# Optimization experiments

Hardware: AMD Instinct MI355X
Metric: run time of the kernel (lower is better)

## Reference

```python
import jax, jax.numpy as jnp
import numpy as np

B, C, T = 4, 768, 512
H, KS, NL, W = 12, 3, 6, 4
D = C // H  # 64


def setup_inputs() -> dict:
    key = jax.random.key(0)
    ks = jax.random.split(key, 24)
    def n(k, shape, scale):
        return jax.random.normal(k, shape, dtype=jnp.float32) * scale
    cscale = C ** -0.5
    return {
        "x": jax.random.normal(ks[0], (B, C, T), dtype=jnp.float32),
        "x_mask": jnp.ones((B, 1, T), dtype=jnp.float32),
        "Wq": n(ks[1], (NL, C, C), cscale), "bq": jnp.zeros((NL, C), jnp.float32),
        "Wk": n(ks[2], (NL, C, C), cscale), "bk": jnp.zeros((NL, C), jnp.float32),
        "Wv": n(ks[3], (NL, C, C), cscale), "bv": jnp.zeros((NL, C), jnp.float32),
        "Wo": n(ks[4], (NL, C, C), cscale), "bo": jnp.zeros((NL, C), jnp.float32),
        "emb_rel_k": n(ks[5], (NL, D, 2 * W + 1), D ** -0.5),
        "emb_rel_v": n(ks[6], (NL, D, 2 * W + 1), D ** -0.5),
        "ffn_w1": n(ks[7], (NL, 4 * C, C, KS), (C * KS) ** -0.5),
        "ffn_b1": jnp.zeros((NL, 4 * C), jnp.float32),
        "ffn_w2": n(ks[8], (NL, C, 4 * C, KS), (4 * C * KS) ** -0.5),
        "ffn_b2": jnp.zeros((NL, C), jnp.float32),
        "norm1_g": jnp.ones((NL, C), jnp.float32), "norm1_b": jnp.zeros((NL, C), jnp.float32),
        "norm2_g": jnp.ones((NL, C), jnp.float32), "norm2_b": jnp.zeros((NL, C), jnp.float32),
    }


def _conv1x1(x, w, b):  # x:[B,C,T] w:[O,C] -> [B,O,T]
    return jnp.einsum('oc,bct->bot', w, x) + b[None, :, None]


def _conv1d(x, w, b, pad):  # x:[B,Ci,T] w:[O,Ci,K]
    y = jax.lax.conv_general_dilated(x, w, (1,), [(pad, pad)],
                                     dimension_numbers=('NCH', 'OIH', 'NCH'))
    return y + b[None, :, None]


def _layer_norm_c(x, g, b):  # normalize over channel dim of [B,C,T]
    m = jnp.mean(x, axis=1, keepdims=True)
    v = jnp.var(x, axis=1, keepdims=True)
    return (x - m) * jax.lax.rsqrt(v + 1e-5) * g[None, :, None] + b[None, :, None]


def _rel_to_abs(x):  # [b,h,l,2l-1] -> [b,h,l,l]
    b, h, l, _ = x.shape
    x = jnp.pad(x, ((0, 0), (0, 0), (0, 0), (0, 1)))
    x = x.reshape(b, h, l * 2 * l)
    x = jnp.pad(x, ((0, 0), (0, 0), (0, l - 1)))
    return x.reshape(b, h, l + 1, 2 * l - 1)[:, :, :l, l - 1:]


def _abs_to_rel(x):  # [b,h,l,l] -> [b,h,l,2l-1]
    b, h, l, _ = x.shape
    x = jnp.pad(x, ((0, 0), (0, 0), (0, 0), (0, l - 1)))
    x = x.reshape(b, h, l * l + l * (l - 1))
    x = jnp.pad(x, ((0, 0), (0, 0), (l, 0)))
    return x.reshape(b, h, l, 2 * l)[:, :, :, 1:]


def _get_rel_emb(emb, t, w):  # emb:[D,2w+1] -> [D,2t-1]
    pad = max(t - (w + 1), 0)
    start = max(w + 1 - t, 0)
    e = jnp.pad(emb, ((0, 0), (pad, pad)))
    return e[:, start:start + 2 * t - 1]


def _attention(x, attn_mask, wq, bq, wk, bk, wv, bv, wo, bo, ek, ev):
    b, c, t = x.shape
    scale = D ** 0.5
    q = _conv1x1(x, wq, bq).reshape(b, H, D, t)
    k = _conv1x1(x, wk, bk).reshape(b, H, D, t)
    v = _conv1x1(x, wv, bv).reshape(b, H, D, t)
    scores = jnp.einsum('bhdt,bhds->bhts', q, k) / scale  # [b,H,t,t]
    k_emb = _get_rel_emb(ek, t, W)  # [D,2t-1]
    rel_logits = jnp.einsum('bhdt,dr->bhtr', q / scale, k_emb)
    scores = scores + _rel_to_abs(rel_logits)
    scores = jnp.where(attn_mask == 0, -10000.0, scores)
    p = jax.nn.softmax(scores, axis=-1)
    out = jnp.einsum('bhts,bhds->bhdt', p, v)
    v_emb = _get_rel_emb(ev, t, W)  # [D,2t-1]
    out = out + jnp.einsum('bhtr,dr->bhdt', _abs_to_rel(p), v_emb)
    return _conv1x1(out.reshape(b, c, t), wo, bo)


def _ffn(x, x_mask, w1, b1, w2, b2):
    y = _conv1d(x * x_mask, w1, b1, KS // 2)
    y = jax.nn.gelu(y, approximate=False)
    y = _conv1d(y * x_mask, w2, b2, KS // 2)
    return y * x_mask


def reference(x, x_mask, Wq, bq, Wk, bk, Wv, bv, Wo, bo, emb_rel_k, emb_rel_v,
              ffn_w1, ffn_b1, ffn_w2, ffn_b2, norm1_g, norm1_b, norm2_g, norm2_b):
    attn_mask = x_mask[:, :, None, :] * x_mask[:, :, :, None]  # [B,1,T,T]
    for i in range(NL):
        y = _attention(x, attn_mask, Wq[i], bq[i], Wk[i], bk[i], Wv[i], bv[i],
                       Wo[i], bo[i], emb_rel_k[i], emb_rel_v[i])
        x = _layer_norm_c(x + y, norm1_g[i], norm1_b[i])
        y = _ffn(x, x_mask, ffn_w1[i], ffn_b1[i], ffn_w2[i], ffn_b2[i])
        x = _layer_norm_c(x + y, norm2_g[i], norm2_b[i])
        x = x * x_mask
    return x
```

## Files before the change

### kernel.cpp

```cpp
#include <hip/hip_runtime.h>
#include <cstddef>

namespace {

constexpr int B  = 4;
constexpr int C  = 768;
constexpr int T  = 512;
constexpr int H  = 12;
constexpr int D  = 64;
constexpr int NL = 6;
constexpr int W  = 4;
constexpr int FF = 3072;

typedef __attribute__((ext_vector_type(8))) short sh8;
typedef __attribute__((ext_vector_type(4))) float f32x4;

__device__ inline float gelu_exact(float x) {
  return 0.5f * x * (1.0f + erff(x * 0.70710678118654752440f));
}
__device__ inline unsigned short f2b(float f) {
  unsigned u = __float_as_uint(f);
  unsigned r = (u + 0x7fffu + ((u >> 16) & 1u)) >> 16;
  return (unsigned short)r;
}
__device__ inline float b2f(unsigned short u) {
  return __uint_as_float((unsigned)u << 16);
}
__device__ inline void gload_lds16(const void* g, void* l) {
  __builtin_amdgcn_global_load_lds(
      (const __attribute__((address_space(1))) unsigned int*)g,
      (__attribute__((address_space(3))) unsigned int*)l, 16, 0, 0);
}

__global__ __launch_bounds__(256) void transpose_cvt_in(
    const float* __restrict__ s, unsigned short* __restrict__ dh,
    float* __restrict__ df)
{
  __shared__ float tile[32][33];
  const int b = blockIdx.z;
  const int c0 = blockIdx.y * 32, t0 = blockIdx.x * 32;
  const int tx = threadIdx.x & 31, ty = threadIdx.x >> 5;
  const float* sp = s + ((size_t)b * C + c0) * T + t0;
#pragma unroll
  for (int i = 0; i < 4; ++i)
    tile[ty + i * 8][tx] = sp[(size_t)(ty + i * 8) * T + tx];
  __syncthreads();
  unsigned short* dph = dh + ((size_t)b * T + t0) * C + c0;
  float* dpf = df + ((size_t)b * T + t0) * C + c0;
#pragma unroll
  for (int i = 0; i < 4; ++i) {
    const float v = tile[tx][ty + i * 8];
    dph[(size_t)(ty + i * 8) * C + tx] = f2b(v);
    dpf[(size_t)(ty + i * 8) * C + tx] = v;
  }
}

__global__ __launch_bounds__(256) void transpose_out(
    const float* __restrict__ s, float* __restrict__ d)
{
  __shared__ float tile[32][33];
  const int b = blockIdx.z;
  const int c0 = blockIdx.y * 32, t0 = blockIdx.x * 32;
  const int tx = threadIdx.x & 31, ty = threadIdx.x >> 5;
  const float* sp = s + ((size_t)b * T + t0) * C + c0;
#pragma unroll
  for (int i = 0; i < 4; ++i)
    tile[ty + i * 8][tx] = sp[(size_t)(ty + i * 8) * C + tx];
  __syncthreads();
  float* dp = d + ((size_t)b * C + c0) * T + t0;
#pragma unroll
  for (int i = 0; i < 4; ++i)
    dp[(size_t)(ty + i * 8) * T + tx] = tile[tx][ty + i * 8];
}

__global__ __launch_bounds__(256) void cvt_qkvo_tiled(
    const float* __restrict__ q, const float* __restrict__ k,
    const float* __restrict__ v, const float* __restrict__ o,
    unsigned short* __restrict__ dq, unsigned short* __restrict__ dk,
    unsigned short* __restrict__ dv, unsigned short* __restrict__ dov)
{
  const int z = blockIdx.y;
  const float* s = z == 0 ? q : z == 1 ? k : z == 2 ? v : o;
  unsigned short* d = z == 0 ? dq : z == 1 ? dk : z == 2 ? dv : dov;
  const int flat = blockIdx.x * 256 + threadIdx.x;
  const int row = flat / (C / 8);
  const int c   = (flat % (C / 8)) * 8;
  const int ks = c >> 5, lhi = (c >> 3) & 3, mt = row >> 4, l15 = row & 15;
  const float* sp = s + (size_t)row * C + c;
  float4 a = *(const float4*)(sp);
  float4 b = *(const float4*)(sp + 4);
  sh8 u;
  u[0] = (short)f2b(a.x); u[1] = (short)f2b(a.y);
  u[2] = (short)f2b(a.z); u[3] = (short)f2b(a.w);
  u[4] = (short)f2b(b.x); u[5] = (short)f2b(b.y);
  u[6] = (short)f2b(b.z); u[7] = (short)f2b(b.w);
  *(sh8*)(d + ((size_t)(mt * (C / 32) + ks) * 64 + lhi * 16 + l15) * 8) = u;
}

__global__ __launch_bounds__(256) void cvt_ffn_tiled(
    const float* __restrict__ s1, const float* __restrict__ s2,
    unsigned short* __restrict__ d1, unsigned short* __restrict__ d2)
{
  const int z = blockIdx.y;
  const float* src = z ? s2 : s1;
  unsigned short* dst = z ? d2 : d1;
  const int O  = z ? C : FF;
  const int Ci = z ? FF : C;
  const int flat = blockIdx.x * 256 + threadIdx.x;
  const int row = flat / (Ci / 8);
  const int c   = (flat % (Ci / 8)) * 8;
  const int ks = c >> 5, lhi = (c >> 3) & 3, mt = row >> 4, l15 = row & 15;
  const float* sp = src + ((size_t)row * Ci + c) * 3;
  float f[24];
#pragma unroll
  for (int i = 0; i < 6; ++i) {
    float4 t4 = *(const float4*)(sp + i * 4);
    f[i * 4 + 0] = t4.x; f[i * 4 + 1] = t4.y; f[i * 4 + 2] = t4.z; f[i * 4 + 3] = t4.w;
  }
  const size_t fragoff =
      ((size_t)(mt * (Ci / 32) + ks) * 64 + lhi * 16 + l15) * 8;
#pragma unroll
  for (int tap = 0; tap < 3; ++tap) {
    sh8 u;
#pragma unroll
    for (int j = 0; j < 8; ++j) u[j] = (short)f2b(f[j * 3 + tap]);
    *(sh8*)(dst + (size_t)tap * O * Ci + fragoff) = u;
  }
}

template <int TAPS, int KSPLIT, bool GELU, bool MASK_OUT, bool OBF16>
__global__ __launch_bounds__(256) void mfma_conv(
    const unsigned short* __restrict__ xin,
    const unsigned short* __restrict__ w0p, const unsigned short* __restrict__ w1p,
    const unsigned short* __restrict__ w2p,
    const float* __restrict__ b0, const float* __restrict__ b1,
    const float* __restrict__ b2,
    const float* __restrict__ mask,
    void* __restrict__ o0p, void* __restrict__ o1p, void* __restrict__ o2p,
    int Cin, int O, int tilesPerPlane, int nz)
{
  constexpr int BN = 64;
  constexpr int ROWS_B = BN + TAPS - 1;
  constexpr int PB = 40;
  __shared__ unsigned short Aw[2][TAPS * 8 * 512];
  __shared__ unsigned short Bx[2][ROWS_B * PB];

  const int nwg = gridDim.x;
  const int orig = blockIdx.x;
  const int wg = (orig & 7) * (nwg >> 3) + (orig >> 3);
  const int txt = wg & 7;
  const int rest = wg >> 3;
  const int zz = rest % nz;
  const int ty = rest / nz;

  const int b  = zz / KSPLIT;
  const int kk = zz % KSPLIT;
  const int TOFF = (TAPS == 3) ? -1 : 0;
  const int t0 = txt * BN;
  const int plane = ty / tilesPerPlane;
  const int mt0 = (ty % tilesPerPlane) * 8;
  const int o0 = mt0 * 16;

  const int tid = threadIdx.x;
  const int lane = tid & 63, wid = tid >> 6;
  const int wm = wid >> 1, wn = wid & 1;
  const int l15 = lane & 15, lhi = lane >> 4;
  const int bmask = b * T;

  const unsigned short* wsel = plane == 0 ? w0p : (plane == 1 ? w1p : w2p);
  const float* bp = plane == 0 ? b0 : (plane == 1 ? b1 : b2);

  const int KST = Cin >> 5;
  const int kchunk = KST / KSPLIT;
  const int ks0 = kk * kchunk, ks1 = ks0 + kchunk;
  const int OT = O >> 4;

  const int brow = tid >> 2, bcl = (tid & 3) << 3;
  const unsigned short* xb_ = xin + (size_t)b * T * Cin;

  sh8 breg, breg2;
  auto stageA = [&](int ks, int buf) {
#pragma unroll
    for (int tap = 0; tap < TAPS; ++tap) {
#pragma unroll
      for (int j = 0; j < 2; ++j) {
        const int rt = wid * 2 + j;
        const unsigned short* src =
            wsel + (((size_t)tap * OT + mt0 + rt) * KST + ks) * 512 + lane * 8;
        gload_lds16(src, &Aw[buf][(tap * 8 + rt) * 512]);
      }
    }
  };
  auto loadB = [&](int ks) {
    const int c0 = ks << 5;
    const unsigned short* xrow = xb_ + c0 + bcl;
    const int tsrc = t0 + brow + TOFF;
    breg = (sh8)0;
    if ((unsigned)tsrc < (unsigned)T)
      breg = *(const sh8*)(xrow + (size_t)tsrc * Cin);
    if constexpr (TAPS == 3) {
      breg2 = (sh8)0;
      if (tid < 8) {
        const int ts2 = t0 + BN + (tid >> 2) + TOFF;
        if ((unsigned)ts2 < (unsigned)T)
          breg2 = *(const sh8*)(xrow + (size_t)ts2 * Cin);
      }
    }
  };
  auto writeB = [&](int buf) {
    *(sh8*)&Bx[buf][brow * PB + bcl] = breg;
    if constexpr (TAPS == 3) {
      if (tid < 8)
        *(sh8*)&Bx[buf][(BN + (tid >> 2)) * PB + bcl] = breg2;
    }
  };

  f32x4 acc[4][2] = {};

  int cur = 0;
  stageA(ks0, 0);
  loadB(ks0);
  writeB(0);
  __syncthreads();

  for (int ks = ks0; ks < ks1; ++ks) {
    const int nxt = cur ^ 1;
    const bool more = (ks + 1 < ks1);
    if (more) { stageA(ks + 1, nxt); loadB(ks + 1); }
#pragma unroll
    for (int tap = 0; tap < TAPS; ++tap) {
      sh8 af[4], bfr[2];
#pragma unroll
      for (int m = 0; m < 4; ++m)
        af[m] = *(const sh8*)&Aw[cur][(tap * 8 + wm * 4 + m) * 512 + lane * 8];
#pragma unroll
      for (int n = 0; n < 2; ++n)
        bfr[n] = *(const sh8*)&Bx[cur][(wn * 32 + n * 16 + l15 + tap) * PB + lhi * 8];
#pragma unroll
      for (int m = 0; m < 4; ++m)
#pragma unroll
        for (int n = 0; n < 2; ++n)
          acc[m][n] = __builtin_amdgcn_mfma_f32_16x16x32_bf16(
              af[m], bfr[n], acc[m][n], 0, 0, 0);
    }
    if (more) writeB(nxt);
    __syncthreads();
    cur = nxt;
  }

  void* obase = plane == 0 ? o0p : (plane == 1 ? o1p : o2p);
  unsigned short* oph = (unsigned short*)obase + (size_t)b * T * O;
  float* opf = (float*)obase + ((size_t)kk * B + b) * (size_t)T * O;
#pragma unroll
  for (int m = 0; m < 4; ++m) {
    const int o = o0 + (wm * 4 + m) * 16 + (lhi << 2);
#pragma unroll
    for (int n = 0; n < 2; ++n) {
      const int t = t0 + wn * 32 + n * 16 + l15;
      const float mk = MASK_OUT ? mask[bmask + t] : 1.f;
      float v[4];
#pragma unroll
      for (int r4 = 0; r4 < 4; ++r4) {
        float x = acc[m][n][r4];
        if (KSPLIT > 1) {
          if (kk == 0) x += bp[o + r4];
        } else {
          x += bp[o + r4];
        }
        if (GELU) x = gelu_exact(x);
        if (MASK_OUT) x *= mk;
        v[r4] = x;
      }
      if constexpr (OBF16) {
        ushort4 hz;
        hz.x = f2b(v[0]); hz.y = f2b(v[1]); hz.z = f2b(v[2]); hz.w = f2b(v[3]);
        *(ushort4*)(oph + (size_t)t * O + o) = hz;
      } else {
        *(float4*)(opf + (size_t)t * O + o) = make_float4(v[0], v[1], v[2], v[3]);
      }
    }
  }
}

__global__ __launch_bounds__(256) void fused_attn(
    const unsigned short* __restrict__ qg,
    const unsigned short* __restrict__ kg,
    const unsigned short* __restrict__ vg,
    const float* __restrict__ mask,
    const float* __restrict__ ek,
    const float* __restrict__ ev,
    unsigned short* __restrict__ outp)
{
  constexpr int PITCH = 72;
  __shared__ unsigned short Qs[64 * PITCH];
  __shared__ unsigned short Ks[2][64 * PITCH];
  __shared__ unsigned short Vs[2][64 * PITCH];
  __shared__ unsigned short Ps[64 * PITCH];
  __shared__ float eks[D * 9], evs[D * 9];
  __shared__ float qekl[64 * 12];
  __shared__ float mks[2][64];

  const int t0 = blockIdx.x * 64;
  const int bh = blockIdx.y;
  const int b = bh / H, h = bh % H;
  const int tid = threadIdx.x;
  const int lane = tid & 63, w = tid >> 6;
  const int l15 = lane & 15, lhi = lane >> 4;

  const size_t base = (size_t)b * T * C + h * D;
  const unsigned short* qh = qg + base;
  const unsigned short* kh = kg + base;
  const unsigned short* vh = vg + base;

  for (int e = tid; e < D * 9; e += 256) { eks[e] = ek[e]; evs[e] = ev[e]; }
  {
    const int tl = tid & 63, d0 = (tid >> 6) << 4;
    const unsigned short* src = qh + (size_t)(t0 + tl) * C + d0;
    *(sh8*)&Qs[tl * PITCH + d0]     = *(const sh8*)(src);
    *(sh8*)&Qs[tl * PITCH + d0 + 8] = *(const sh8*)(src + 8);
  }
  __syncthreads();
  {
    const int tl = tid & 63, g = tid >> 6;
    for (int j = g; j < 9; j += 4) {
      float a = 0.f;
      for (int d = 0; d < D; ++d)
        a = fmaf(b2f(Qs[tl * PITCH + d]), eks[d * 9 + j], a);
      qekl[tl * 12 + j] = a * 0.125f;
    }
  }
  const int t_loc = w * 16 + l15;
  const int t = t0 + t_loc;
  const float mask_t = mask[b * T + t];
  const sh8 bq0 = *(const sh8*)&Qs[t_loc * PITCH + lhi * 8];
  const sh8 bq1 = *(const sh8*)&Qs[t_loc * PITCH + 32 + lhi * 8];

  const int sl = tid & 63, d0s = (tid >> 6) << 4;
  {
    const unsigned short* srck = kh + (size_t)sl * C + d0s;
    *(sh8*)&Ks[0][sl * PITCH + d0s]     = *(const sh8*)(srck);
    *(sh8*)&Ks[0][sl * PITCH + d0s + 8] = *(const sh8*)(srck + 8);
    const unsigned short* srcv = vh + (size_t)sl * C + d0s;
    sh8 u0 = *(const sh8*)(srcv);
    sh8 u1 = *(const sh8*)(srcv + 8);
#pragma unroll
    for (int j = 0; j < 8; ++j) Vs[0][(d0s + j) * PITCH + sl] = (unsigned short)u0[j];
#pragma unroll
    for (int j = 0; j < 8; ++j) Vs[0][(d0s + 8 + j) * PITCH + sl] = (unsigned short)u1[j];
    if (tid < 64) mks[0][tid] = mask[b * T + tid];
  }
  __syncthreads();

  float m_run = -1e30f, l_run = 0.f;
  f32x4 oacc[4] = {};
  int cur = 0;
  sh8 kr0, kr1, vr0, vr1;
  float mkr = 0.f;

  for (int s0 = 0; s0 < T; s0 += 64) {
    const int nxt = cur ^ 1;
    const bool more = (s0 + 64 < T);
    if (more) {
      const unsigned short* srck = kh + (size_t)(s0 + 64 + sl) * C + d0s;
      kr0 = *(const sh8*)(srck);
      kr1 = *(const sh8*)(srck + 8);
      const unsigned short* srcv = vh + (size_t)(s0 + 64 + sl) * C + d0s;
      vr0 = *(const sh8*)(srcv);
      vr1 = *(const sh8*)(srcv + 8);
      if (tid < 64) mkr = mask[b * T + s0 + 64 + tid];
    }

    float p[16];
#pragma unroll
    for (int n = 0; n < 4; ++n) {
      const sh8 a0 = *(const sh8*)&Ks[cur][(n * 16 + l15) * PITCH + lhi * 8];
      const sh8 a1 = *(const sh8*)&Ks[cur][(n * 16 + l15) * PITCH + 32 + lhi * 8];
      f32x4 acc = {};
      acc = __builtin_amdgcn_mfma_f32_16x16x32_bf16(a0, bq0, acc, 0, 0, 0);
      acc = __builtin_amdgcn_mfma_f32_16x16x32_bf16(a1, bq1, acc, 0, 0, 0);
#pragma unroll
      for (int r = 0; r < 4; ++r) {
        const int s = s0 + n * 16 + lhi * 4 + r;
        float v = acc[r] * 0.125f;
        const int j = s - t + 4;
        if ((unsigned)j < 9u) v += qekl[t_loc * 12 + j];
        if (mask_t * mks[cur][s - s0] == 0.f) v = -10000.0f;
        p[n * 4 + r] = v;
      }
    }
    float mloc = p[0];
#pragma unroll
    for (int i = 1; i < 16; ++i) mloc = fmaxf(mloc, p[i]);
    mloc = fmaxf(mloc, __shfl_xor(mloc, 16));
    mloc = fmaxf(mloc, __shfl_xor(mloc, 32));
    const float m_new = fmaxf(m_run, mloc);
    const float f = __expf(m_run - m_new);
    float sloc = 0.f;
#pragma unroll
    for (int i = 0; i < 16; ++i) { p[i] = __expf(p[i] - m_new); sloc += p[i]; }
    sloc += __shfl_xor(sloc, 16);
    sloc += __shfl_xor(sloc, 32);
    l_run = l_run * f + sloc;
    m_run = m_new;
#pragma unroll
    for (int m = 0; m < 4; ++m)
#pragma unroll
      for (int r = 0; r < 4; ++r) oacc[m][r] *= f;
#pragma unroll
    for (int n = 0; n < 4; ++n) {
      uint2 pk;
      pk.x = (unsigned)f2b(p[n * 4 + 0]) | ((unsigned)f2b(p[n * 4 + 1]) << 16);
      pk.y = (unsigned)f2b(p[n * 4 + 2]) | ((unsigned)f2b(p[n * 4 + 3]) << 16);
      *(uint2*)&Ps[t_loc * PITCH + n * 16 + lhi * 4] = pk;
    }
    asm volatile("s_waitcnt lgkmcnt(0)" ::: "memory");
    const sh8 bp0 = *(const sh8*)&Ps[t_loc * PITCH + lhi * 8];
    const sh8 bp1 = *(const sh8*)&Ps[t_loc * PITCH + 32 + lhi * 8];
#pragma unroll
    for (int m = 0; m < 4; ++m) {
      const sh8 a0 = *(const sh8*)&Vs[cur][(m * 16 + l15) * PITCH + lhi * 8];
      const sh8 a1 = *(const sh8*)&Vs[cur][(m * 16 + l15) * PITCH + 32 + lhi * 8];
      oacc[m] = __builtin_amdgcn_mfma_f32_16x16x32_bf16(a0, bp0, oacc[m], 0, 0, 0);
      oacc[m] = __builtin_amdgcn_mfma_f32_16x16x32_bf16(a1, bp1, oacc[m], 0, 0, 0);
    }
    if (t + 4 >= s0 && t < s0 + 68) {
#pragma unroll
      for (int j = 0; j < 9; ++j) {
        const int s = t + j - 4;
        if (s >= s0 && s < s0 + 64) {
          const float pv = b2f(Ps[t_loc * PITCH + (s - s0)]);
#pragma unroll
          for (int m = 0; m < 4; ++m)
#pragma unroll
            for (int r = 0; r < 4; ++r)
              oacc[m][r] = fmaf(pv, evs[(m * 16 + lhi * 4 + r) * 9 + j], oacc[m][r]);
        }
      }
    }
    if (more) {
      *(sh8*)&Ks[nxt][sl * PITCH + d0s]     = kr0;
      *(sh8*)&Ks[nxt][sl * PITCH + d0s + 8] = kr1;
#pragma unroll
      for (int j = 0; j < 8; ++j) Vs[nxt][(d0s + j) * PITCH + sl] = (unsigned short)vr0[j];
#pragma unroll
      for (int j = 0; j < 8; ++j) Vs[nxt][(d0s + 8 + j) * PITCH + sl] = (unsigned short)vr1[j];
      if (tid < 64) mks[nxt][tid] = mkr;
    }
    __syncthreads();
    cur = nxt;
  }
  const float invl = 1.f / l_run;
  unsigned short* ob = outp + (size_t)(b * T + t) * C + h * D;
#pragma unroll
  for (int m = 0; m < 4; ++m) {
    ushort4 hz;
    hz.x = f2b(oacc[m][0] * invl);
    hz.y = f2b(oacc[m][1] * invl);
    hz.z = f2b(oacc[m][2] * invl);
    hz.w = f2b(oacc[m][3] * invl);
    *(ushort4*)(ob + m * 16 + lhi * 4) = hz;
  }
}

template <int NP, bool MASKY, bool MASKF>
__global__ __launch_bounds__(256) void add_norm_wave(
    const float* __restrict__ xr, const float* __restrict__ ypart,
    const float* __restrict__ g, const float* __restrict__ bta,
    const float* __restrict__ mask, float* __restrict__ dst,
    unsigned short* __restrict__ dsth)
{
  const int b = blockIdx.y;
  const int t = blockIdx.x * 4 + (threadIdx.x >> 6);
  const int lane = threadIdx.x & 63;
  const float mkt = mask[b * T + t];
  const size_t rowoff = ((size_t)b * T + t) * C;
  const int ci0 = lane * 12;

  float vv[12];
  float sum = 0.f, sq = 0.f;
#pragma unroll
  for (int q = 0; q < 3; ++q) {
    const int ci = ci0 + q * 4;
    float4 xv = *(const float4*)(xr + rowoff + ci);
    float4 yv = make_float4(0.f, 0.f, 0.f, 0.f);
#pragma unroll
    for (int p = 0; p < NP; ++p) {
      float4 t4 = *(const float4*)(ypart + (size_t)p * B * T * C + rowoff + ci);
      yv.x += t4.x; yv.y += t4.y; yv.z += t4.z; yv.w += t4.w;
    }
    if (MASKY) { yv.x *= mkt; yv.y *= mkt; yv.z *= mkt; yv.w *= mkt; }
    const float v0 = xv.x + yv.x, v1 = xv.y + yv.y;
    const float v2 = xv.z + yv.z, v3 = xv.w + yv.w;
    vv[q * 4 + 0] = v0; vv[q * 4 + 1] = v1; vv[q * 4 + 2] = v2; vv[q * 4 + 3] = v3;
    sum += v0 + v1 + v2 + v3;
    sq = fmaf(v0, v0, fmaf(v1, v1, fmaf(v2, v2, fmaf(v3, v3, sq))));
  }
#pragma unroll
  for (int o = 32; o > 0; o >>= 1) {
    sum += __shfl_xor(sum, o);
    sq += __shfl_xor(sq, o);
  }
  const float m = sum * (1.f / C);
  const float rs = rsqrtf(sq * (1.f / C) - m * m + 1e-5f);
#pragma unroll
  for (int q = 0; q < 3; ++q) {
    const int ci = ci0 + q * 4;
    float4 gv = *(const float4*)(g + ci);
    float4 bv = *(const float4*)(bta + ci);
    float o0 = (vv[q * 4 + 0] - m) * rs * gv.x + bv.x;
    float o1 = (vv[q * 4 + 1] - m) * rs * gv.y + bv.y;
    float o2 = (vv[q * 4 + 2] - m) * rs * gv.z + bv.z;
    float o3 = (vv[q * 4 + 3] - m) * rs * gv.w + bv.w;
    if (MASKF) { o0 *= mkt; o1 *= mkt; o2 *= mkt; o3 *= mkt; }
    *(float4*)(dst + rowoff + ci) = make_float4(o0, o1, o2, o3);
    const float hm = MASKF ? 1.f : mkt;
    ushort4 hz;
    hz.x = f2b(o0 * hm); hz.y = f2b(o1 * hm); hz.z = f2b(o2 * hm); hz.w = f2b(o3 * hm);
    *(ushort4*)(dsth + rowoff + ci) = hz;
  }
}

}

extern "C" void kernel_launch(void* const* d_in, const int* in_sizes, int n_in,
                              void* d_out, int out_size, void* d_ws, size_t ws_size,
                              hipStream_t stream) {
  const float* x_in = (const float*)d_in[0];
  const float* mask = (const float*)d_in[1];
  const float* Wq = (const float*)d_in[2];
  const float* bq = (const float*)d_in[3];
  const float* Wk = (const float*)d_in[4];
  const float* bk = (const float*)d_in[5];
  const float* Wv = (const float*)d_in[6];
  const float* bv = (const float*)d_in[7];
  const float* Wo = (const float*)d_in[8];
  const float* bo = (const float*)d_in[9];
  const float* ek = (const float*)d_in[10];
  const float* ev = (const float*)d_in[11];
  const float* w1 = (const float*)d_in[12];
  const float* b1 = (const float*)d_in[13];
  const float* w2 = (const float*)d_in[14];
  const float* b2 = (const float*)d_in[15];
  const float* n1g = (const float*)d_in[16];
  const float* n1b = (const float*)d_in[17];
  const float* n2g = (const float*)d_in[18];
  const float* n2b = (const float*)d_in[19];

  float* ws = (float*)d_ws;
  const size_t SZ_X = (size_t)B * C * T;
  float* xr    = ws;
  float* xr1   = xr + SZ_X;
  float* ypart = xr1 + SZ_X;
  unsigned short* xbh = (unsigned short*)(ypart + 4 * SZ_X);
  unsigned short* xfh = xbh + SZ_X;
  unsigned short* qbh = xfh + SZ_X;
  unsigned short* kbh = qbh + SZ_X;
  unsigned short* vbh = kbh + SZ_X;
  unsigned short* hidh = vbh + SZ_X;
  unsigned short* w1t = hidh + (size_t)B * FF * T;
  unsigned short* w2t = w1t + (size_t)3 * FF * C;
  unsigned short* wqt = w2t + (size_t)3 * FF * C;
  unsigned short* wkt = wqt + (size_t)C * C;
  unsigned short* wvt = wkt + (size_t)C * C;
  unsigned short* wot = wvt + (size_t)C * C;
  float* outp = (float*)d_out;

  const dim3 blk(256);
  transpose_cvt_in<<<dim3(T / 32, C / 32, B), blk, 0, stream>>>(x_in, xbh, xr);

  for (int i = 0; i < NL; ++i) {
    const size_t wOff = (size_t)i * C * C;
    cvt_qkvo_tiled<<<dim3((C * C / 8) / 256, 4), blk, 0, stream>>>(
        Wq + wOff, Wk + wOff, Wv + wOff, Wo + wOff, wqt, wkt, wvt, wot);
    cvt_ffn_tiled<<<dim3((FF * C / 8) / 256, 2), blk, 0, stream>>>(
        w1 + (size_t)i * FF * C * 3, w2 + (size_t)i * C * FF * 3, w1t, w2t);
    mfma_conv<1, 1, false, false, true><<<dim3(8 * 18 * 4), blk, 0, stream>>>(
        xbh, wqt, wkt, wvt, bq + i * C, bk + i * C, bv + i * C, mask,
        qbh, kbh, vbh, C, C, 6, 4);
    fused_attn<<<dim3(T / 64, B * H), blk, 0, stream>>>(
        qbh, kbh, vbh, mask, ek + (size_t)i * D * 9, ev + (size_t)i * D * 9, hidh);
    mfma_conv<1, 3, false, false, false><<<dim3(8 * 6 * 12), blk, 0, stream>>>(
        hidh, wot, wot, wot, bo + i * C, bo + i * C, bo + i * C, mask,
        ypart, ypart, ypart, C, C, 6, 12);
    add_norm_wave<3, false, false><<<dim3(T / 4, B), blk, 0, stream>>>(
        xr, ypart, n1g + i * C, n1b + i * C, mask, xr1, xfh);
    mfma_conv<3, 1, true, true, true><<<dim3(8 * 24 * 4), blk, 0, stream>>>(
        xfh, w1t, w1t, w1t, b1 + i * FF, b1 + i * FF, b1 + i * FF, mask,
        hidh, hidh, hidh, C, FF, 24, 4);
    mfma_conv<3, 4, false, false, false><<<dim3(8 * 6 * 16), blk, 0, stream>>>(
        hidh, w2t, w2t, w2t, b2 + i * C, b2 + i * C, b2 + i * C, mask,
        ypart, ypart, ypart, FF, C, 6, 16);
    add_norm_wave<4, true, true><<<dim3(T / 4, B), blk, 0, stream>>>(
        xr1, ypart, n2g + i * C, n2b + i * C, mask, xr, xbh);
  }
  transpose_out<<<dim3(T / 32, C / 32, B), blk, 0, stream>>>(xr, outp);
}
```

Before: 1.327 ms.

## Batch weight conversion across layers and widen FFN conv time tiles to 128

Moves the per-layer bf16 weight conversion kernels out of the layer loop into single launches covering all layers, storing converted weights for every layer in the workspace. Adds a BN template parameter to the MFMA conv kernel and uses 128-wide time tiles for both FFN convolutions, so each wave computes more output columns per loaded weight fragment. This reduces kernel launch count and increases A-operand reuse, at the cost of more accumulator registers, fewer workgroups and a larger workspace footprint.

```diff
diff --git a/kernel.cpp b/kernel.cpp
--- a/kernel.cpp
+++ b/kernel.cpp
@@ -80,8 +80,9 @@
     unsigned short* __restrict__ dv, unsigned short* __restrict__ dov)
 {
   const int z = blockIdx.y;
-  const float* s = z == 0 ? q : z == 1 ? k : z == 2 ? v : o;
-  unsigned short* d = z == 0 ? dq : z == 1 ? dk : z == 2 ? dv : dov;
+  const size_t loff = (size_t)blockIdx.z * C * C;
+  const float* s = (z == 0 ? q : z == 1 ? k : z == 2 ? v : o) + loff;
+  unsigned short* d = (z == 0 ? dq : z == 1 ? dk : z == 2 ? dv : dov) + loff;
   const int flat = blockIdx.x * 256 + threadIdx.x;
   const int row = flat / (C / 8);
   const int c   = (flat % (C / 8)) * 8;
@@ -102,8 +103,9 @@
     unsigned short* __restrict__ d1, unsigned short* __restrict__ d2)
 {
   const int z = blockIdx.y;
-  const float* src = z ? s2 : s1;
-  unsigned short* dst = z ? d2 : d1;
+  const int layer = blockIdx.z;
+  const float* src = (z ? s2 : s1) + (size_t)layer * FF * C * 3;
+  unsigned short* dst = (z ? d2 : d1) + (size_t)layer * 3 * FF * C;
   const int O  = z ? C : FF;
   const int Ci = z ? FF : C;
   const int flat = blockIdx.x * 256 + threadIdx.x;
@@ -128,7 +130,7 @@
   }
 }
 
-template <int TAPS, int KSPLIT, bool GELU, bool MASK_OUT, bool OBF16>
+template <int TAPS, int BN, int KSPLIT, bool GELU, bool MASK_OUT, bool OBF16>
 __global__ __launch_bounds__(256) void mfma_conv(
     const unsigned short* __restrict__ xin,
     const unsigned short* __restrict__ w0p, const unsigned short* __restrict__ w1p,
@@ -139,17 +141,19 @@
     void* __restrict__ o0p, void* __restrict__ o1p, void* __restrict__ o2p,
     int Cin, int O, int tilesPerPlane, int nz)
 {
-  constexpr int BN = 64;
   constexpr int ROWS_B = BN + TAPS - 1;
   constexpr int PB = 40;
+  constexpr int NPASS = BN / 64;
+  constexpr int NF = BN / 32;
+  constexpr int NT = T / BN;
   __shared__ unsigned short Aw[2][TAPS * 8 * 512];
   __shared__ unsigned short Bx[2][ROWS_B * PB];
 
   const int nwg = gridDim.x;
   const int orig = blockIdx.x;
   const int wg = (orig & 7) * (nwg >> 3) + (orig >> 3);
-  const int txt = wg & 7;
-  const int rest = wg >> 3;
+  const int txt = wg % NT;
+  const int rest = wg / NT;
   const int zz = rest % nz;
   const int ty = rest / nz;
 
@@ -175,10 +179,9 @@
   const int ks0 = kk * kchunk, ks1 = ks0 + kchunk;
   const int OT = O >> 4;
 
-  const int brow = tid >> 2, bcl = (tid & 3) << 3;
   const unsigned short* xb_ = xin + (size_t)b * T * Cin;
 
-  sh8 breg, breg2;
+  sh8 breg[NPASS], breg2;
   auto stageA = [&](int ks, int buf) {
 #pragma unroll
     for (int tap = 0; tap < TAPS; ++tap) {
@@ -193,29 +196,38 @@
   };
   auto loadB = [&](int ks) {
     const int c0 = ks << 5;
-    const unsigned short* xrow = xb_ + c0 + bcl;
-    const int tsrc = t0 + brow + TOFF;
-    breg = (sh8)0;
-    if ((unsigned)tsrc < (unsigned)T)
-      breg = *(const sh8*)(xrow + (size_t)tsrc * Cin);
+#pragma unroll
+    for (int p = 0; p < NPASS; ++p) {
+      const int idx = tid + p * 256;
+      const int row = idx >> 2, c8 = (idx & 3) << 3;
+      const int tsrc = t0 + row + TOFF;
+      breg[p] = (sh8)0;
+      if ((unsigned)tsrc < (unsigned)T)
+        breg[p] = *(const sh8*)(xb_ + (size_t)tsrc * Cin + c0 + c8);
+    }
     if constexpr (TAPS == 3) {
       breg2 = (sh8)0;
       if (tid < 8) {
-        const int ts2 = t0 + BN + (tid >> 2) + TOFF;
+        const int row = BN + (tid >> 2), c8 = (tid & 3) << 3;
+        const int ts2 = t0 + row + TOFF;
         if ((unsigned)ts2 < (unsigned)T)
-          breg2 = *(const sh8*)(xrow + (size_t)ts2 * Cin);
+          breg2 = *(const sh8*)(xb_ + (size_t)ts2 * Cin + c0 + c8);
       }
     }
   };
   auto writeB = [&](int buf) {
-    *(sh8*)&Bx[buf][brow * PB + bcl] = breg;
+#pragma unroll
+    for (int p = 0; p < NPASS; ++p) {
+      const int idx = tid + p * 256;
+      *(sh8*)&Bx[buf][(idx >> 2) * PB + ((idx & 3) << 3)] = breg[p];
+    }
     if constexpr (TAPS == 3) {
       if (tid < 8)
-        *(sh8*)&Bx[buf][(BN + (tid >> 2)) * PB + bcl] = breg2;
+        *(sh8*)&Bx[buf][(BN + (tid >> 2)) * PB + ((tid & 3) << 3)] = breg2;
     }
   };
 
-  f32x4 acc[4][2] = {};
+  f32x4 acc[4][NF] = {};
 
   int cur = 0;
   stageA(ks0, 0);
@@ -229,17 +241,17 @@
     if (more) { stageA(ks + 1, nxt); loadB(ks + 1); }
 #pragma unroll
     for (int tap = 0; tap < TAPS; ++tap) {
-      sh8 af[4], bfr[2];
+      sh8 af[4], bfr[NF];
 #pragma unroll
       for (int m = 0; m < 4; ++m)
         af[m] = *(const sh8*)&Aw[cur][(tap * 8 + wm * 4 + m) * 512 + lane * 8];
 #pragma unroll
-      for (int n = 0; n < 2; ++n)
-        bfr[n] = *(const sh8*)&Bx[cur][(wn * 32 + n * 16 + l15 + tap) * PB + lhi * 8];
+      for (int n = 0; n < NF; ++n)
+        bfr[n] = *(const sh8*)&Bx[cur][(wn * (NF * 16) + n * 16 + l15 + tap) * PB + lhi * 8];
 #pragma unroll
       for (int m = 0; m < 4; ++m)
 #pragma unroll
-        for (int n = 0; n < 2; ++n)
+        for (int n = 0; n < NF; ++n)
           acc[m][n] = __builtin_amdgcn_mfma_f32_16x16x32_bf16(
               af[m], bfr[n], acc[m][n], 0, 0, 0);
     }
@@ -255,8 +267,8 @@
   for (int m = 0; m < 4; ++m) {
     const int o = o0 + (wm * 4 + m) * 16 + (lhi << 2);
 #pragma unroll
-    for (int n = 0; n < 2; ++n) {
-      const int t = t0 + wn * 32 + n * 16 + l15;
+    for (int n = 0; n < NF; ++n) {
+      const int t = t0 + wn * (NF * 16) + n * 16 + l15;
       const float mk = MASK_OUT ? mask[bmask + t] : 1.f;
       float v[4];
 #pragma unroll
@@ -548,6 +560,7 @@
 
   float* ws = (float*)d_ws;
   const size_t SZ_X = (size_t)B * C * T;
+  const size_t SZ_W1 = (size_t)3 * FF * C;
   float* xr    = ws;
   float* xr1   = xr + SZ_X;
   float* ypart = xr1 + SZ_X;
@@ -558,37 +571,41 @@
   unsigned short* vbh = kbh + SZ_X;
   unsigned short* hidh = vbh + SZ_X;
   unsigned short* w1t = hidh + (size_t)B * FF * T;
-  unsigned short* w2t = w1t + (size_t)3 * FF * C;
-  unsigned short* wqt = w2t + (size_t)3 * FF * C;
-  unsigned short* wkt = wqt + (size_t)C * C;
-  unsigned short* wvt = wkt + (size_t)C * C;
-  unsigned short* wot = wvt + (size_t)C * C;
+  unsigned short* w2t = w1t + (size_t)NL * SZ_W1;
+  unsigned short* wqt = w2t + (size_t)NL * SZ_W1;
+  unsigned short* wkt = wqt + (size_t)NL * C * C;
+  unsigned short* wvt = wkt + (size_t)NL * C * C;
+  unsigned short* wot = wvt + (size_t)NL * C * C;
   float* outp = (float*)d_out;
 
   const dim3 blk(256);
   transpose_cvt_in<<<dim3(T / 32, C / 32, B), blk, 0, stream>>>(x_in, xbh, xr);
+  cvt_qkvo_tiled<<<dim3((C * C / 8) / 256, 4, NL), blk, 0, stream>>>(
+      Wq, Wk, Wv, Wo, wqt, wkt, wvt, wot);
+  cvt_ffn_tiled<<<dim3((FF * C / 8) / 256, 2, NL), blk, 0, stream>>>(
+      w1, w2, w1t, w2t);
 
   for (int i = 0; i < NL; ++i) {
     const size_t wOff = (size_t)i * C * C;
-    cvt_qkvo_tiled<<<dim3((C * C / 8) / 256, 4), blk, 0, stream>>>(
-        Wq + wOff, Wk + wOff, Wv + wOff, Wo + wOff, wqt, wkt, wvt, wot);
-    cvt_ffn_tiled<<<dim3((FF * C / 8) / 256, 2), blk, 0, stream>>>(
-        w1 + (size_t)i * FF * C * 3, w2 + (size_t)i * C * FF * 3, w1t, w2t);
-    mfma_conv<1, 1, false, false, true><<<dim3(8 * 18 * 4), blk, 0, stream>>>(
-        xbh, wqt, wkt, wvt, bq + i * C, bk + i * C, bv + i * C, mask,
+    const unsigned short* w1l = w1t + (size_t)i * SZ_W1;
+    const unsigned short* w2l = w2t + (size_t)i * SZ_W1;
+    mfma_conv<1, 64, 1, false, false, true><<<dim3(8 * 18 * 4), blk, 0, stream>>>(
+        xbh, wqt + wOff, wkt + wOff, wvt + wOff,
+        bq + i * C, bk + i * C, bv + i * C, mask,
         qbh, kbh, vbh, C, C, 6, 4);
     fused_attn<<<dim3(T / 64, B * H), blk, 0, stream>>>(
         qbh, kbh, vbh, mask, ek + (size_t)i * D * 9, ev + (size_t)i * D * 9, hidh);
-    mfma_conv<1, 3, false, false, false><<<dim3(8 * 6 * 12), blk, 0, stream>>>(
-        hidh, wot, wot, wot, bo + i * C, bo + i * C, bo + i * C, mask,
+    mfma_conv<1, 64, 3, false, false, false><<<dim3(8 * 6 * 12), blk, 0, stream>>>(
+        hidh, wot + wOff, wot + wOff, wot + wOff,
+        bo + i * C, bo + i * C, bo + i * C, mask,
         ypart, ypart, ypart, C, C, 6, 12);
     add_norm_wave<3, false, false><<<dim3(T / 4, B), blk, 0, stream>>>(
         xr, ypart, n1g + i * C, n1b + i * C, mask, xr1, xfh);
-    mfma_conv<3, 1, true, true, true><<<dim3(8 * 24 * 4), blk, 0, stream>>>(
-        xfh, w1t, w1t, w1t, b1 + i * FF, b1 + i * FF, b1 + i * FF, mask,
+    mfma_conv<3, 128, 1, true, true, true><<<dim3(4 * 24 * 4), blk, 0, stream>>>(
+        xfh, w1l, w1l, w1l, b1 + i * FF, b1 + i * FF, b1 + i * FF, mask,
         hidh, hidh, hidh, C, FF, 24, 4);
-    mfma_conv<3, 4, false, false, false><<<dim3(8 * 6 * 16), blk, 0, stream>>>(
-        hidh, w2t, w2t, w2t, b2 + i * C, b2 + i * C, b2 + i * C, mask,
+    mfma_conv<3, 128, 4, false, false, false><<<dim3(4 * 6 * 16), blk, 0, stream>>>(
+        hidh, w2l, w2l, w2l, b2 + i * C, b2 + i * C, b2 + i * C, mask,
         ypart, ypart, ypart, FF, C, 6, 16);
     add_norm_wave<4, true, true><<<dim3(T / 4, B), blk, 0, stream>>>(
         xr1, ypart, n2g + i * C, n2b + i * C, mask, xr, xbh);
```

Measured after the change: 1.275 ms. 1.04x faster.
